# Optimization experiments

Measured on AMD Instinct MI355X. Metric: run time of the kernel, lower is better.

The kernel has to match this reference:

```python
import jax, jax.numpy as jnp
import numpy as np

NEG_SLOPE = 0.2  # PyG GATConv default

def gat_conv(x, src, dst, W, att_src, att_dst, bias, n_nodes):
    """PyG-style GATConv (self-loops already included in src/dst)."""
    H, C = att_src.shape
    h = (x @ W).reshape(n_nodes, H, C)                       # [N,H,C]
    a_src = jnp.einsum('nhc,hc->nh', h, att_src)             # [N,H]
    a_dst = jnp.einsum('nhc,hc->nh', h, att_dst)             # [N,H]
    e = jax.nn.leaky_relu(a_src[src] + a_dst[dst], NEG_SLOPE)  # [E,H]
    # numerically stable segment softmax over incoming edges of each dst node
    e_max = jax.ops.segment_max(e, dst, num_segments=n_nodes)   # [N,H]
    e_exp = jnp.exp(e - e_max[dst])
    denom = jax.ops.segment_sum(e_exp, dst, num_segments=n_nodes)  # [N,H]
    alpha = e_exp / (denom[dst] + 1e-16)                     # [E,H]
    msg = h[src] * alpha[:, :, None]                         # [E,H,C]
    out = jax.ops.segment_sum(msg, dst, num_segments=n_nodes)  # [N,H,C]
    return out.reshape(n_nodes, H * C) + bias

def add_self_loops(edge_index, n_nodes):
    loop = jnp.arange(n_nodes, dtype=edge_index.dtype)
    src = jnp.concatenate([edge_index[0], loop])
    dst = jnp.concatenate([edge_index[1], loop])
    return src, dst

def setup_inputs() -> dict:
    key = jax.random.key(0)
    ks = jax.random.split(key, 12)
    N, E, IN, HID, H1 = 50000, 800000, 128, 64, 4
    s = lambda k, shape, scale: jax.random.normal(k, shape, dtype=jnp.float32) * scale
    return {
        'x': s(ks[0], (N, IN), 1.0),
        'edge_index': jax.random.randint(ks[1], (2, E), 0, N, dtype=jnp.int64),
        'W1': s(ks[2], (IN, H1 * HID), (2.0 / IN) ** 0.5),
        'att_src1': s(ks[3], (H1, HID), 0.1),
        'att_dst1': s(ks[4], (H1, HID), 0.1),
        'b1': s(ks[5], (H1 * HID,), 0.02),
        'W2': s(ks[6], (H1 * HID, HID), (2.0 / (H1 * HID)) ** 0.5),
        'att_src2': s(ks[7], (1, HID), 0.1),
        'att_dst2': s(ks[8], (1, HID), 0.1),
        'b2': s(ks[9], (HID,), 0.02),
        'Ws': s(ks[10], (HID, 1), (2.0 / HID) ** 0.5),
        'bs': s(ks[11], (1,), 0.02),
    }

def reference(x, edge_index, W1, att_src1, att_dst1, b1, W2, att_src2, att_dst2, b2, Ws, bs):
    N = x.shape[0]
    src, dst = add_self_loops(edge_index, N)
    h = jax.nn.elu(gat_conv(x, src, dst, W1, att_src1, att_dst1, b1, N))   # [N,256]
    # dropout is identity in eval mode
    h = jax.nn.elu(gat_conv(h, src, dst, W2, att_src2, att_dst2, b2, N))   # [N,64]
    scores = (h @ Ws + bs).squeeze(-1)                                     # [N]
    return h, scores
```

## Files before the change

kernel.cpp:

```cpp
#include <hip/hip_runtime.h>
#include <hip/hip_bf16.h>
#include <math.h>


#define LRELU_SLOPE 0.2f

typedef __attribute__((ext_vector_type(8))) short short8;
typedef __attribute__((ext_vector_type(4))) float f32x4;

__device__ inline ushort f2bf(float f) {
    uint u = __float_as_uint(f);
    return (ushort)((u + 0x7FFFu + ((u >> 16) & 1u)) >> 16);
}
__device__ inline float bf2f(ushort u) {
    return __uint_as_float(((uint)u) << 16);
}

__global__ __launch_bounds__(256)
void conv_bf16(const float* __restrict__ in, ushort* __restrict__ out, int n)
{
    int i = (blockIdx.x * blockDim.x + threadIdx.x) << 2;
    if (i >= n) return;
    float4 v = *(const float4*)(in + i);
    ushort4 o;
    o.x = f2bf(v.x); o.y = f2bf(v.y); o.z = f2bf(v.z); o.w = f2bf(v.w);
    *(ushort4*)(out + i) = o;
}

__global__ __launch_bounds__(256)
void prefrag(const float* __restrict__ W, ushort* __restrict__ out,
             int J, int T, int ldn)
{
    int tid = blockIdx.x * blockDim.x + threadIdx.x;
    if (tid >= J * T * 64) return;
    int l = tid & 63, jt = tid >> 6;
    int t = jt % T, j = jt / T;
    int n = j * 16 + (l & 15);
    int k0 = t * 32 + (l >> 4) * 8;
    ushort o[8];
    #pragma unroll
    for (int b = 0; b < 8; ++b) o[b] = f2bf(W[(size_t)(k0 + b) * ldn + n]);
    *(short8*)(out + (size_t)tid * 8) = *(short8*)o;
}

template<int J, int T, int H>
__global__ __launch_bounds__(256)
void gemm_mfma(const ushort* __restrict__ A, const ushort* __restrict__ Bf,
               ushort* __restrict__ Cbf, const float* __restrict__ attS,
               const float* __restrict__ attD, float* __restrict__ as_,
               float* __restrict__ ad_, int M)
{
    constexpr int K = 32 * T;
    constexpr int NN = 16 * J;
    const int l = threadIdx.x & 63;
    const int wid = blockIdx.x * (blockDim.x >> 6) + (threadIdx.x >> 6);
    const int base = wid * 16;
    if (base >= M) return;
    const int lm = l & 15, lg = l >> 4;

    short8 a[T];
    const ushort* ap = A + (size_t)(base + lm) * K + lg * 8;
    #pragma unroll
    for (int t = 0; t < T; ++t) a[t] = *(const short8*)(ap + t * 32);

    f32x4 acc[J];
    #pragma unroll
    for (int j = 0; j < J; ++j) acc[j] = (f32x4){0.f, 0.f, 0.f, 0.f};

    const ushort* bp = Bf + (size_t)l * 8;
    #pragma unroll
    for (int j = 0; j < J; ++j)
        #pragma unroll
        for (int t = 0; t < T; ++t) {
            short8 b = *(const short8*)(bp + (size_t)(j * T + t) * 512);
            acc[j] = __builtin_amdgcn_mfma_f32_16x16x32_bf16(a[t], b, acc[j], 0, 0, 0);
        }

    float sp[H][4], dp[H][4];
    #pragma unroll
    for (int h = 0; h < H; ++h)
        #pragma unroll
        for (int r = 0; r < 4; ++r) { sp[h][r] = 0.f; dp[h][r] = 0.f; }

    #pragma unroll
    for (int j = 0; j < J; ++j) {
        const int h = j / (J / H);
        const int coff = (j % (J / H)) * 16 + lm;
        float ws = attS[h * 64 + coff];
        float wd = attD[h * 64 + coff];
        #pragma unroll
        for (int r = 0; r < 4; ++r) {
            int row = base + lg * 4 + r;
            Cbf[(size_t)row * NN + j * 16 + lm] = f2bf(acc[j][r]);
            sp[h][r] = fmaf(acc[j][r], ws, sp[h][r]);
            dp[h][r] = fmaf(acc[j][r], wd, dp[h][r]);
        }
    }
    #pragma unroll
    for (int h = 0; h < H; ++h)
        #pragma unroll
        for (int r = 0; r < 4; ++r) {
            float s = sp[h][r], d = dp[h][r];
            s += __shfl_xor(s, 1); d += __shfl_xor(d, 1);
            s += __shfl_xor(s, 2); d += __shfl_xor(d, 2);
            s += __shfl_xor(s, 4); d += __shfl_xor(d, 4);
            s += __shfl_xor(s, 8); d += __shfl_xor(d, 8);
            if (lm == 0) {
                int row = base + lg * 4 + r;
                as_[row * H + h] = s;
                ad_[row * H + h] = d;
            }
        }
}

__global__ __launch_bounds__(256)
void degree_hist(const int* __restrict__ edst, int* __restrict__ deg, int E)
{
    int i = blockIdx.x * blockDim.x + threadIdx.x;
    if (i < E) atomicAdd(&deg[edst[i]], 1);
}

__global__ __launch_bounds__(1024)
void scan_rowptr(const int* __restrict__ deg, int* __restrict__ rowptr,
                 int* __restrict__ cursor, int N)
{
    __shared__ int wsums[16];
    __shared__ int s_carry;
    const int tid = threadIdx.x, lane = tid & 63, wid = tid >> 6;
    if (tid == 0) s_carry = 0;
    __syncthreads();
    const int N4 = N >> 2;
    for (int base = 0; base < N4; base += 1024) {
        int i4 = base + tid;
        int4 v = (i4 < N4) ? ((const int4*)deg)[i4] : make_int4(0, 0, 0, 0);
        int tsum = v.x + v.y + v.z + v.w;
        int sc = tsum;
        #pragma unroll
        for (int off = 1; off < 64; off <<= 1) {
            int t = __shfl_up(sc, off);
            if (lane >= off) sc += t;
        }
        if (lane == 63) wsums[wid] = sc;
        __syncthreads();
        if (wid == 0) {
            int wv = (lane < 16) ? wsums[lane] : 0;
            #pragma unroll
            for (int off = 1; off < 16; off <<= 1) {
                int t = __shfl_up(wv, off);
                if (lane >= off) wv += t;
            }
            if (lane < 16) wsums[lane] = wv;
        }
        __syncthreads();
        int wbase = (wid > 0) ? wsums[wid - 1] : 0;
        int excl = s_carry + wbase + sc - tsum;
        if (i4 < N4) {
            int4 o;
            o.x = excl; o.y = excl + v.x; o.z = o.y + v.y; o.w = o.z + v.z;
            ((int4*)rowptr)[i4] = o;
            ((int4*)cursor)[i4] = make_int4(0, 0, 0, 0);
        }
        __syncthreads();
        if (tid == 0) s_carry += wsums[15];
        __syncthreads();
    }
    if (tid == 0) rowptr[N] = s_carry;
}

__global__ __launch_bounds__(256)
void scatter_edges(const int* __restrict__ esrc, const int* __restrict__ edst,
                   const int* __restrict__ rowptr, int* __restrict__ cursor,
                   int* __restrict__ csr_src, int E)
{
    int i = blockIdx.x * blockDim.x + threadIdx.x;
    if (i >= E) return;
    int s = esrc[i], d = edst[i];
    int pos = rowptr[d] + atomicAdd(&cursor[d], 1);
    csr_src[pos] = s;
}

__global__ __launch_bounds__(256)
void aggregate_l1(const int* __restrict__ rowptr, const int* __restrict__ csr_src,
                  const ushort* __restrict__ h1, const float* __restrict__ as_,
                  const float* __restrict__ ad_, const float* __restrict__ bias,
                  ushort* __restrict__ outbf, int N)
{
    int w = (blockIdx.x * blockDim.x + threadIdx.x) >> 6;
    int lane = threadIdx.x & 63;
    if (w >= N) return;
    const int head = lane >> 4;
    const int c0 = lane << 2;
    const float ad = ad_[w * 4 + head];
    float4 acc = make_float4(0.f, 0.f, 0.f, 0.f);
    float dsum = 0.f;

    {
        float el = as_[w * 4 + head] + ad;
        el = el > 0.f ? el : LRELU_SLOPE * el;
        float p = __expf(el);
        ushort4 u = *(const ushort4*)(h1 + (size_t)w * 256 + c0);
        acc.x = p * bf2f(u.x); acc.y = p * bf2f(u.y);
        acc.z = p * bf2f(u.z); acc.w = p * bf2f(u.w);
        dsum = p;
    }

    int e = rowptr[w];
    const int e1 = rowptr[w + 1];
    for (; e + 3 < e1; e += 4) {
        int s0 = csr_src[e], s1 = csr_src[e + 1];
        int s2 = csr_src[e + 2], s3 = csr_src[e + 3];
        float e0 = as_[s0 * 4 + head] + ad, e1v = as_[s1 * 4 + head] + ad;
        float e2 = as_[s2 * 4 + head] + ad, e3 = as_[s3 * 4 + head] + ad;
        e0 = e0 > 0.f ? e0 : LRELU_SLOPE * e0;
        e1v = e1v > 0.f ? e1v : LRELU_SLOPE * e1v;
        e2 = e2 > 0.f ? e2 : LRELU_SLOPE * e2;
        e3 = e3 > 0.f ? e3 : LRELU_SLOPE * e3;
        float p0 = __expf(e0), p1 = __expf(e1v);
        float p2 = __expf(e2), p3 = __expf(e3);
        ushort4 u0 = *(const ushort4*)(h1 + (size_t)s0 * 256 + c0);
        ushort4 u1 = *(const ushort4*)(h1 + (size_t)s1 * 256 + c0);
        ushort4 u2 = *(const ushort4*)(h1 + (size_t)s2 * 256 + c0);
        ushort4 u3 = *(const ushort4*)(h1 + (size_t)s3 * 256 + c0);
        acc.x = fmaf(p0, bf2f(u0.x), acc.x); acc.y = fmaf(p0, bf2f(u0.y), acc.y);
        acc.z = fmaf(p0, bf2f(u0.z), acc.z); acc.w = fmaf(p0, bf2f(u0.w), acc.w);
        acc.x = fmaf(p1, bf2f(u1.x), acc.x); acc.y = fmaf(p1, bf2f(u1.y), acc.y);
        acc.z = fmaf(p1, bf2f(u1.z), acc.z); acc.w = fmaf(p1, bf2f(u1.w), acc.w);
        acc.x = fmaf(p2, bf2f(u2.x), acc.x); acc.y = fmaf(p2, bf2f(u2.y), acc.y);
        acc.z = fmaf(p2, bf2f(u2.z), acc.z); acc.w = fmaf(p2, bf2f(u2.w), acc.w);
        acc.x = fmaf(p3, bf2f(u3.x), acc.x); acc.y = fmaf(p3, bf2f(u3.y), acc.y);
        acc.z = fmaf(p3, bf2f(u3.z), acc.z); acc.w = fmaf(p3, bf2f(u3.w), acc.w);
        dsum += (p0 + p1) + (p2 + p3);
    }
    for (; e < e1; ++e) {
        int s0 = csr_src[e];
        float e0 = as_[s0 * 4 + head] + ad;
        e0 = e0 > 0.f ? e0 : LRELU_SLOPE * e0;
        float p0 = __expf(e0);
        ushort4 u0 = *(const ushort4*)(h1 + (size_t)s0 * 256 + c0);
        acc.x = fmaf(p0, bf2f(u0.x), acc.x); acc.y = fmaf(p0, bf2f(u0.y), acc.y);
        acc.z = fmaf(p0, bf2f(u0.z), acc.z); acc.w = fmaf(p0, bf2f(u0.w), acc.w);
        dsum += p0;
    }
    const float inv = 1.f / (dsum + 1e-16f);
    const float4 b = *(const float4*)(bias + c0);
    float ox = acc.x * inv + b.x; ox = ox > 0.f ? ox : expm1f(ox);
    float oy = acc.y * inv + b.y; oy = oy > 0.f ? oy : expm1f(oy);
    float oz = acc.z * inv + b.z; oz = oz > 0.f ? oz : expm1f(oz);
    float ow = acc.w * inv + b.w; ow = ow > 0.f ? ow : expm1f(ow);
    ushort4 o;
    o.x = f2bf(ox); o.y = f2bf(oy); o.z = f2bf(oz); o.w = f2bf(ow);
    *(ushort4*)(outbf + (size_t)w * 256 + c0) = o;
}

__global__ __launch_bounds__(256)
void aggregate_l2(const int* __restrict__ rowptr, const int* __restrict__ csr_src,
                  const ushort* __restrict__ h2, const float* __restrict__ as_,
                  const float* __restrict__ ad_, const float* __restrict__ b2,
                  const float* __restrict__ Wsv, const float* __restrict__ bs,
                  float* __restrict__ hout, float* __restrict__ scores, int N)
{
    int w = (blockIdx.x * blockDim.x + threadIdx.x) >> 6;
    int lane = threadIdx.x & 63;
    if (w >= N) return;
    const float ad = ad_[w];
    float acc, dsum;
    {
        float el = as_[w] + ad;
        el = el > 0.f ? el : LRELU_SLOPE * el;
        float p = __expf(el);
        acc = p * bf2f(h2[(size_t)w * 64 + lane]);
        dsum = p;
    }
    int e = rowptr[w];
    const int e1 = rowptr[w + 1];
    for (; e + 3 < e1; e += 4) {
        int s0 = csr_src[e], s1 = csr_src[e + 1];
        int s2 = csr_src[e + 2], s3 = csr_src[e + 3];
        float e0 = as_[s0] + ad, e1v = as_[s1] + ad;
        float e2 = as_[s2] + ad, e3 = as_[s3] + ad;
        e0 = e0 > 0.f ? e0 : LRELU_SLOPE * e0;
        e1v = e1v > 0.f ? e1v : LRELU_SLOPE * e1v;
        e2 = e2 > 0.f ? e2 : LRELU_SLOPE * e2;
        e3 = e3 > 0.f ? e3 : LRELU_SLOPE * e3;
        float p0 = __expf(e0), p1 = __expf(e1v);
        float p2 = __expf(e2), p3 = __expf(e3);
        acc = fmaf(p0, bf2f(h2[(size_t)s0 * 64 + lane]), acc);
        acc = fmaf(p1, bf2f(h2[(size_t)s1 * 64 + lane]), acc);
        acc = fmaf(p2, bf2f(h2[(size_t)s2 * 64 + lane]), acc);
        acc = fmaf(p3, bf2f(h2[(size_t)s3 * 64 + lane]), acc);
        dsum += (p0 + p1) + (p2 + p3);
    }
    for (; e < e1; ++e) {
        int s0 = csr_src[e];
        float e0 = as_[s0] + ad;
        e0 = e0 > 0.f ? e0 : LRELU_SLOPE * e0;
        float p0 = __expf(e0);
        acc = fmaf(p0, bf2f(h2[(size_t)s0 * 64 + lane]), acc);
        dsum += p0;
    }
    float v = acc / (dsum + 1e-16f) + b2[lane];
    v = v > 0.f ? v : expm1f(v);
    hout[(size_t)w * 64 + lane] = v;
    float sc = v * Wsv[lane];
    #pragma unroll
    for (int off = 32; off; off >>= 1) sc += __shfl_down(sc, off);
    if (lane == 0) scores[w] = sc + bs[0];
}

extern "C" void kernel_launch(void* const* d_in, const int* in_sizes, int n_in,
                              void* d_out, int out_size, void* d_ws, size_t ws_size,
                              hipStream_t stream)
{
    const float* x    = (const float*)d_in[0];
    const int*   ei   = (const int*)d_in[1];
    const float* W1   = (const float*)d_in[2];
    const float* as1w = (const float*)d_in[3];
    const float* ad1w = (const float*)d_in[4];
    const float* b1   = (const float*)d_in[5];
    const float* W2   = (const float*)d_in[6];
    const float* as2w = (const float*)d_in[7];
    const float* ad2w = (const float*)d_in[8];
    const float* b2   = (const float*)d_in[9];
    const float* Ws   = (const float*)d_in[10];
    const float* bs   = (const float*)d_in[11];

    const int N  = in_sizes[0] / 128;
    const int E  = in_sizes[1] / 2;
    const int* esrc = ei;
    const int* edst = ei + E;

    ushort* h1bf  = (ushort*)d_ws;
    ushort* hl1bf = h1bf + (size_t)N * 256;
    ushort* xbf   = hl1bf + (size_t)N * 256;
    ushort* h2bf  = xbf + (size_t)N * 128;
    ushort* bfr1  = h2bf + (size_t)N * 64;
    ushort* bfr2  = bfr1 + 32768;
    float*  as1   = (float*)(bfr2 + 16384);
    float*  ad1   = as1 + (size_t)N * 4;
    float*  as2   = ad1 + (size_t)N * 4;
    float*  ad2   = as2 + N;
    int*    deg    = (int*)(ad2 + N);
    int*    cursor = deg + N;
    int*    rowptr = cursor + N;
    int*    csr_src= rowptr + N + 4;

    float* hout   = (float*)d_out;
    float* scores = hout + (size_t)N * 64;

    hipMemsetAsync(deg, 0, (size_t)N * sizeof(int), stream);
    degree_hist<<<(E + 255) / 256, 256, 0, stream>>>(edst, deg, E);
    scan_rowptr<<<1, 1024, 0, stream>>>(deg, rowptr, cursor, N);
    scatter_edges<<<(E + 255) / 256, 256, 0, stream>>>(
        esrc, edst, rowptr, cursor, csr_src, E);

    conv_bf16<<<((size_t)N * 128 / 4 + 255) / 256, 256, 0, stream>>>(
        x, xbf, N * 128);
    prefrag<<<(16 * 4 * 64 + 255) / 256, 256, 0, stream>>>(W1, bfr1, 16, 4, 256);
    prefrag<<<(4 * 8 * 64 + 255) / 256, 256, 0, stream>>>(W2, bfr2, 4, 8, 64);

    gemm_mfma<16, 4, 4><<<(N / 16 + 3) / 4, 256, 0, stream>>>(
        xbf, bfr1, h1bf, as1w, ad1w, as1, ad1, N);
    aggregate_l1<<<((size_t)N * 64 + 255) / 256, 256, 0, stream>>>(
        rowptr, csr_src, h1bf, as1, ad1, b1, hl1bf, N);

    gemm_mfma<4, 8, 1><<<(N / 16 + 3) / 4, 256, 0, stream>>>(
        hl1bf, bfr2, h2bf, as2w, ad2w, as2, ad2, N);
    aggregate_l2<<<((size_t)N * 64 + 255) / 256, 256, 0, stream>>>(
        rowptr, csr_src, h2bf, as2, ad2, b2, Ws, bs, hout, scores, N);
}
```

Measured before the change: 256.5 us.

## Fuse fp32-to-bf16 conversion into GEMM and precompute per-edge attention coefficients

Removes the standalone x-to-bf16 conversion kernel by converting fp32 inputs inside the first GEMM's A-operand load. Adds csr_dst output to the edge scatter and new per-edge kernels that compute leaky-relu/exp attention weights once per edge and head. The aggregation kernels then read these coefficients contiguously instead of gathering source scores and recomputing exp in every lane. This trades redundant transcendental work for extra kernel launches and writing and reading sizeable per-edge coefficient buffers.

```diff
diff --git a/kernel.cpp b/kernel.cpp
--- a/kernel.cpp
+++ b/kernel.cpp
@@ -14,17 +14,6 @@
 }
 __device__ inline float bf2f(ushort u) {
     return __uint_as_float(((uint)u) << 16);
-}
-
-__global__ __launch_bounds__(256)
-void conv_bf16(const float* __restrict__ in, ushort* __restrict__ out, int n)
-{
-    int i = (blockIdx.x * blockDim.x + threadIdx.x) << 2;
-    if (i >= n) return;
-    float4 v = *(const float4*)(in + i);
-    ushort4 o;
-    o.x = f2bf(v.x); o.y = f2bf(v.y); o.z = f2bf(v.z); o.w = f2bf(v.w);
-    *(ushort4*)(out + i) = o;
 }
 
 __global__ __launch_bounds__(256)
@@ -43,9 +32,9 @@
     *(short8*)(out + (size_t)tid * 8) = *(short8*)o;
 }
 
-template<int J, int T, int H>
-__global__ __launch_bounds__(256)
-void gemm_mfma(const ushort* __restrict__ A, const ushort* __restrict__ Bf,
+template<int J, int T, int H, bool AF32>
+__global__ __launch_bounds__(256)
+void gemm_mfma(const void* __restrict__ Araw, const ushort* __restrict__ Bf,
                ushort* __restrict__ Cbf, const float* __restrict__ attS,
                const float* __restrict__ attD, float* __restrict__ as_,
                float* __restrict__ ad_, int M)
@@ -59,9 +48,22 @@
     const int lm = l & 15, lg = l >> 4;
 
     short8 a[T];
-    const ushort* ap = A + (size_t)(base + lm) * K + lg * 8;
-    #pragma unroll
-    for (int t = 0; t < T; ++t) a[t] = *(const short8*)(ap + t * 32);
+    if constexpr (AF32) {
+        const float* ap = (const float*)Araw + (size_t)(base + lm) * K + lg * 8;
+        #pragma unroll
+        for (int t = 0; t < T; ++t) {
+            float4 v0 = *(const float4*)(ap + t * 32);
+            float4 v1 = *(const float4*)(ap + t * 32 + 4);
+            ushort o[8];
+            o[0] = f2bf(v0.x); o[1] = f2bf(v0.y); o[2] = f2bf(v0.z); o[3] = f2bf(v0.w);
+            o[4] = f2bf(v1.x); o[5] = f2bf(v1.y); o[6] = f2bf(v1.z); o[7] = f2bf(v1.w);
+            a[t] = *(short8*)o;
+        }
+    } else {
+        const ushort* ap = (const ushort*)Araw + (size_t)(base + lm) * K + lg * 8;
+        #pragma unroll
+        for (int t = 0; t < T; ++t) a[t] = *(const short8*)(ap + t * 32);
+    }
 
     f32x4 acc[J];
     #pragma unroll
@@ -170,32 +172,62 @@
 __global__ __launch_bounds__(256)
 void scatter_edges(const int* __restrict__ esrc, const int* __restrict__ edst,
                    const int* __restrict__ rowptr, int* __restrict__ cursor,
-                   int* __restrict__ csr_src, int E)
+                   int* __restrict__ csr_src, int* __restrict__ csr_dst, int E)
 {
     int i = blockIdx.x * blockDim.x + threadIdx.x;
     if (i >= E) return;
     int s = esrc[i], d = edst[i];
     int pos = rowptr[d] + atomicAdd(&cursor[d], 1);
     csr_src[pos] = s;
+    csr_dst[pos] = d;
+}
+
+__global__ __launch_bounds__(256)
+void edge_coef_l1(const int* __restrict__ csr_src, const int* __restrict__ csr_dst,
+                  const float* __restrict__ as_, const float* __restrict__ ad_,
+                  float* __restrict__ p1, int E)
+{
+    int i = blockIdx.x * blockDim.x + threadIdx.x;
+    if (i >= E) return;
+    int s = csr_src[i], d = csr_dst[i];
+    float4 a = *(const float4*)(as_ + (size_t)s * 4);
+    float4 b = *(const float4*)(ad_ + (size_t)d * 4);
+    float4 o;
+    float e0 = a.x + b.x; e0 = e0 > 0.f ? e0 : LRELU_SLOPE * e0; o.x = __expf(e0);
+    float e1 = a.y + b.y; e1 = e1 > 0.f ? e1 : LRELU_SLOPE * e1; o.y = __expf(e1);
+    float e2 = a.z + b.z; e2 = e2 > 0.f ? e2 : LRELU_SLOPE * e2; o.z = __expf(e2);
+    float e3 = a.w + b.w; e3 = e3 > 0.f ? e3 : LRELU_SLOPE * e3; o.w = __expf(e3);
+    *(float4*)(p1 + (size_t)i * 4) = o;
+}
+
+__global__ __launch_bounds__(256)
+void edge_coef_l2(const int* __restrict__ csr_src, const int* __restrict__ csr_dst,
+                  const float* __restrict__ as_, const float* __restrict__ ad_,
+                  float* __restrict__ p2, int E)
+{
+    int i = blockIdx.x * blockDim.x + threadIdx.x;
+    if (i >= E) return;
+    float e0 = as_[csr_src[i]] + ad_[csr_dst[i]];
+    e0 = e0 > 0.f ? e0 : LRELU_SLOPE * e0;
+    p2[i] = __expf(e0);
 }
 
 __global__ __launch_bounds__(256)
 void aggregate_l1(const int* __restrict__ rowptr, const int* __restrict__ csr_src,
-                  const ushort* __restrict__ h1, const float* __restrict__ as_,
-                  const float* __restrict__ ad_, const float* __restrict__ bias,
-                  ushort* __restrict__ outbf, int N)
+                  const float* __restrict__ p1, const ushort* __restrict__ h1,
+                  const float* __restrict__ as_, const float* __restrict__ ad_,
+                  const float* __restrict__ bias, ushort* __restrict__ outbf, int N)
 {
     int w = (blockIdx.x * blockDim.x + threadIdx.x) >> 6;
     int lane = threadIdx.x & 63;
     if (w >= N) return;
     const int head = lane >> 4;
     const int c0 = lane << 2;
-    const float ad = ad_[w * 4 + head];
-    float4 acc = make_float4(0.f, 0.f, 0.f, 0.f);
-    float dsum = 0.f;
+    float4 acc;
+    float dsum;
 
     {
-        float el = as_[w * 4 + head] + ad;
+        float el = as_[w * 4 + head] + ad_[w * 4 + head];
         el = el > 0.f ? el : LRELU_SLOPE * el;
         float p = __expf(el);
         ushort4 u = *(const ushort4*)(h1 + (size_t)w * 256 + c0);
@@ -207,35 +239,29 @@
     int e = rowptr[w];
     const int e1 = rowptr[w + 1];
     for (; e + 3 < e1; e += 4) {
-        int s0 = csr_src[e], s1 = csr_src[e + 1];
+        int s0 = csr_src[e],     s1 = csr_src[e + 1];
         int s2 = csr_src[e + 2], s3 = csr_src[e + 3];
-        float e0 = as_[s0 * 4 + head] + ad, e1v = as_[s1 * 4 + head] + ad;
-        float e2 = as_[s2 * 4 + head] + ad, e3 = as_[s3 * 4 + head] + ad;
-        e0 = e0 > 0.f ? e0 : LRELU_SLOPE * e0;
-        e1v = e1v > 0.f ? e1v : LRELU_SLOPE * e1v;
-        e2 = e2 > 0.f ? e2 : LRELU_SLOPE * e2;
-        e3 = e3 > 0.f ? e3 : LRELU_SLOPE * e3;
-        float p0 = __expf(e0), p1 = __expf(e1v);
-        float p2 = __expf(e2), p3 = __expf(e3);
+        float p0 = p1[(size_t)(e + 0) * 4 + head];
+        float p1v = p1[(size_t)(e + 1) * 4 + head];
+        float p2 = p1[(size_t)(e + 2) * 4 + head];
+        float p3 = p1[(size_t)(e + 3) * 4 + head];
         ushort4 u0 = *(const ushort4*)(h1 + (size_t)s0 * 256 + c0);
         ushort4 u1 = *(const ushort4*)(h1 + (size_t)s1 * 256 + c0);
         ushort4 u2 = *(const ushort4*)(h1 + (size_t)s2 * 256 + c0);
         ushort4 u3 = *(const ushort4*)(h1 + (size_t)s3 * 256 + c0);
         acc.x = fmaf(p0, bf2f(u0.x), acc.x); acc.y = fmaf(p0, bf2f(u0.y), acc.y);
         acc.z = fmaf(p0, bf2f(u0.z), acc.z); acc.w = fmaf(p0, bf2f(u0.w), acc.w);
-        acc.x = fmaf(p1, bf2f(u1.x), acc.x); acc.y = fmaf(p1, bf2f(u1.y), acc.y);
-        acc.z = fmaf(p1, bf2f(u1.z), acc.z); acc.w = fmaf(p1, bf2f(u1.w), acc.w);
+        acc.x = fmaf(p1v, bf2f(u1.x), acc.x); acc.y = fmaf(p1v, bf2f(u1.y), acc.y);
+        acc.z = fmaf(p1v, bf2f(u1.z), acc.z); acc.w = fmaf(p1v, bf2f(u1.w), acc.w);
         acc.x = fmaf(p2, bf2f(u2.x), acc.x); acc.y = fmaf(p2, bf2f(u2.y), acc.y);
         acc.z = fmaf(p2, bf2f(u2.z), acc.z); acc.w = fmaf(p2, bf2f(u2.w), acc.w);
         acc.x = fmaf(p3, bf2f(u3.x), acc.x); acc.y = fmaf(p3, bf2f(u3.y), acc.y);
         acc.z = fmaf(p3, bf2f(u3.z), acc.z); acc.w = fmaf(p3, bf2f(u3.w), acc.w);
-        dsum += (p0 + p1) + (p2 + p3);
+        dsum += (p0 + p1v) + (p2 + p3);
     }
     for (; e < e1; ++e) {
         int s0 = csr_src[e];
-        float e0 = as_[s0 * 4 + head] + ad;
-        e0 = e0 > 0.f ? e0 : LRELU_SLOPE * e0;
-        float p0 = __expf(e0);
+        float p0 = p1[(size_t)e * 4 + head];
         ushort4 u0 = *(const ushort4*)(h1 + (size_t)s0 * 256 + c0);
         acc.x = fmaf(p0, bf2f(u0.x), acc.x); acc.y = fmaf(p0, bf2f(u0.y), acc.y);
         acc.z = fmaf(p0, bf2f(u0.z), acc.z); acc.w = fmaf(p0, bf2f(u0.w), acc.w);
@@ -254,18 +280,18 @@
 
 __global__ __launch_bounds__(256)
 void aggregate_l2(const int* __restrict__ rowptr, const int* __restrict__ csr_src,
-                  const ushort* __restrict__ h2, const float* __restrict__ as_,
-                  const float* __restrict__ ad_, const float* __restrict__ b2,
-                  const float* __restrict__ Wsv, const float* __restrict__ bs,
-                  float* __restrict__ hout, float* __restrict__ scores, int N)
+                  const float* __restrict__ p2, const ushort* __restrict__ h2,
+                  const float* __restrict__ as_, const float* __restrict__ ad_,
+                  const float* __restrict__ b2, const float* __restrict__ Wsv,
+                  const float* __restrict__ bs, float* __restrict__ hout,
+                  float* __restrict__ scores, int N)
 {
     int w = (blockIdx.x * blockDim.x + threadIdx.x) >> 6;
     int lane = threadIdx.x & 63;
     if (w >= N) return;
-    const float ad = ad_[w];
     float acc, dsum;
     {
-        float el = as_[w] + ad;
+        float el = as_[w] + ad_[w];
         el = el > 0.f ? el : LRELU_SLOPE * el;
         float p = __expf(el);
         acc = p * bf2f(h2[(size_t)w * 64 + lane]);
@@ -274,27 +300,18 @@
     int e = rowptr[w];
     const int e1 = rowptr[w + 1];
     for (; e + 3 < e1; e += 4) {
-        int s0 = csr_src[e], s1 = csr_src[e + 1];
+        int s0 = csr_src[e],     s1 = csr_src[e + 1];
         int s2 = csr_src[e + 2], s3 = csr_src[e + 3];
-        float e0 = as_[s0] + ad, e1v = as_[s1] + ad;
-        float e2 = as_[s2] + ad, e3 = as_[s3] + ad;
-        e0 = e0 > 0.f ? e0 : LRELU_SLOPE * e0;
-        e1v = e1v > 0.f ? e1v : LRELU_SLOPE * e1v;
-        e2 = e2 > 0.f ? e2 : LRELU_SLOPE * e2;
-        e3 = e3 > 0.f ? e3 : LRELU_SLOPE * e3;
-        float p0 = __expf(e0), p1 = __expf(e1v);
-        float p2 = __expf(e2), p3 = __expf(e3);
+        float p0 = p2[e], p1 = p2[e + 1], p2v = p2[e + 2], p3 = p2[e + 3];
         acc = fmaf(p0, bf2f(h2[(size_t)s0 * 64 + lane]), acc);
         acc = fmaf(p1, bf2f(h2[(size_t)s1 * 64 + lane]), acc);
-        acc = fmaf(p2, bf2f(h2[(size_t)s2 * 64 + lane]), acc);
+        acc = fmaf(p2v, bf2f(h2[(size_t)s2 * 64 + lane]), acc);
         acc = fmaf(p3, bf2f(h2[(size_t)s3 * 64 + lane]), acc);
-        dsum += (p0 + p1) + (p2 + p3);
+        dsum += (p0 + p1) + (p2v + p3);
     }
     for (; e < e1; ++e) {
         int s0 = csr_src[e];
-        float e0 = as_[s0] + ad;
-        e0 = e0 > 0.f ? e0 : LRELU_SLOPE * e0;
-        float p0 = __expf(e0);
+        float p0 = p2[e];
         acc = fmaf(p0, bf2f(h2[(size_t)s0 * 64 + lane]), acc);
         dsum += p0;
     }
@@ -331,18 +348,20 @@
 
     ushort* h1bf  = (ushort*)d_ws;
     ushort* hl1bf = h1bf + (size_t)N * 256;
-    ushort* xbf   = hl1bf + (size_t)N * 256;
-    ushort* h2bf  = xbf + (size_t)N * 128;
+    ushort* h2bf  = hl1bf + (size_t)N * 256;
     ushort* bfr1  = h2bf + (size_t)N * 64;
     ushort* bfr2  = bfr1 + 32768;
     float*  as1   = (float*)(bfr2 + 16384);
     float*  ad1   = as1 + (size_t)N * 4;
     float*  as2   = ad1 + (size_t)N * 4;
     float*  ad2   = as2 + N;
-    int*    deg    = (int*)(ad2 + N);
+    float*  p1    = ad2 + N;
+    float*  p2    = p1 + (size_t)E * 4;
+    int*    deg    = (int*)(p2 + E);
     int*    cursor = deg + N;
     int*    rowptr = cursor + N;
     int*    csr_src= rowptr + N + 4;
+    int*    csr_dst= csr_src + E;
 
     float* hout   = (float*)d_out;
     float* scores = hout + (size_t)N * 64;
@@ -351,20 +370,22 @@
     degree_hist<<<(E + 255) / 256, 256, 0, stream>>>(edst, deg, E);
     scan_rowptr<<<1, 1024, 0, stream>>>(deg, rowptr, cursor, N);
     scatter_edges<<<(E + 255) / 256, 256, 0, stream>>>(
-        esrc, edst, rowptr, cursor, csr_src, E);
-
-    conv_bf16<<<((size_t)N * 128 / 4 + 255) / 256, 256, 0, stream>>>(
-        x, xbf, N * 128);
+        esrc, edst, rowptr, cursor, csr_src, csr_dst, E);
+
     prefrag<<<(16 * 4 * 64 + 255) / 256, 256, 0, stream>>>(W1, bfr1, 16, 4, 256);
     prefrag<<<(4 * 8 * 64 + 255) / 256, 256, 0, stream>>>(W2, bfr2, 4, 8, 64);
 
-    gemm_mfma<16, 4, 4><<<(N / 16 + 3) / 4, 256, 0, stream>>>(
-        xbf, bfr1, h1bf, as1w, ad1w, as1, ad1, N);
+    gemm_mfma<16, 4, 4, true><<<(N / 16 + 3) / 4, 256, 0, stream>>>(
+        x, bfr1, h1bf, as1w, ad1w, as1, ad1, N);
+    edge_coef_l1<<<(E + 255) / 256, 256, 0, stream>>>(
+        csr_src, csr_dst, as1, ad1, p1, E);
     aggregate_l1<<<((size_t)N * 64 + 255) / 256, 256, 0, stream>>>(
-        rowptr, csr_src, h1bf, as1, ad1, b1, hl1bf, N);
-
-    gemm_mfma<4, 8, 1><<<(N / 16 + 3) / 4, 256, 0, stream>>>(
+        rowptr, csr_src, p1, h1bf, as1, ad1, b1, hl1bf, N);
+
+    gemm_mfma<4, 8, 1, false><<<(N / 16 + 3) / 4, 256, 0, stream>>>(
         hl1bf, bfr2, h2bf, as2w, ad2w, as2, ad2, N);
+    edge_coef_l2<<<(E + 255) / 256, 256, 0, stream>>>(
+        csr_src, csr_dst, as2, ad2, p2, E);
     aggregate_l2<<<((size_t)N * 64 + 255) / 256, 256, 0, stream>>>(
-        rowptr, csr_src, h2bf, as2, ad2, b2, Ws, bs, hout, scores, N);
-}
+        rowptr, csr_src, p2, h2bf, as2, ad2, b2, Ws, bs, hout, scores, N);
+}
```

After: 266.2 us. 1.04x slower.
